# Kernel optimization log

Hardware: AMD Instinct MI355X
Metric: run time of the kernel (lower is better)

## Reference

```python
import jax, jax.numpy as jnp
import numpy as np

N = 100_000      # total nodes (1000 graphs x 100 nodes)
E = 1_600_000    # total edges (avg degree 16)
B = 1_000        # ego nodes == batch size
IN_G, HID, H1, HFC, HMLP = 16, 64, 3, 128, 128
D_SENS, D_TGT, D_AREA = 64, 32, 32
OUT_S, OUT_C = 6, 8


def _seg_softmax(e, dst, n):
    # softmax over incoming edges of each destination node; e: [E,H,1]
    m = jax.ops.segment_max(e, dst, num_segments=n)
    ex = jnp.exp(e - m[dst])
    s = jax.ops.segment_sum(ex, dst, num_segments=n)
    return ex / s[dst]


def _egat(feat, efeat, src, dst, Wni, Wnj, Wfij, Wnode, attn, bias, H, d_node, d_edge):
    # DGL EGATConv: f_out = leaky_relu(f_ni[src] + f_nj[dst] + f_fij + bias)
    n = feat.shape[0]
    f_ni = feat @ Wni.T                      # [N, H*d_edge]
    f_nj = feat @ Wnj.T                      # [N, H*d_edge]
    f_e = efeat @ Wfij.T                     # [E, H*d_edge]
    f_out = f_ni[src] + f_nj[dst] + f_e + bias
    f_out = jax.nn.leaky_relu(f_out, 0.01).reshape(-1, H, d_edge)
    e = (f_out * attn).sum(-1, keepdims=True)   # [E,H,1]
    a = _seg_softmax(e, dst, n)                  # edge softmax by dst
    ft = (feat @ Wnode.T).reshape(n, H, d_node)
    h = jax.ops.segment_sum(ft[src] * a, dst, num_segments=n)  # [N,H,d_node]
    return h, f_out


def _ln(x, gamma, beta, eps=1e-5):
    mu = x.mean(-1, keepdims=True)
    v = ((x - mu) ** 2).mean(-1, keepdims=True)
    return (x - mu) * jax.lax.rsqrt(v + eps) * gamma + beta


def setup_inputs() -> dict:
    key = jax.random.key(0)
    ks = jax.random.split(key, 30)
    ego_idx = jnp.arange(0, N, N // B, dtype=jnp.int32)   # one ego node per graph
    feat = jax.random.normal(ks[0], (N, IN_G), jnp.float32)
    feat = feat.at[:, 5].set(0.0).at[ego_idx, 5].set(1.0)  # ego flag column
    enorm = jax.random.uniform(ks[1], (E, 1), dtype=jnp.float32)
    src = jax.random.randint(ks[2], (E,), 0, N, jnp.int32)
    dst = jax.random.randint(ks[3], (E,), 0, N, jnp.int32)
    sensor = jax.random.normal(ks[4], (B, D_SENS), jnp.float32)
    target = jax.random.normal(ks[5], (B, 1, D_TGT), jnp.float32)
    area = jax.random.normal(ks[6], (B, 1, D_AREA), jnp.float32)

    def w(k, o, i):
        return jax.random.normal(k, (o, i), jnp.float32) / np.sqrt(i).astype(np.float32)

    p = {
        'Wni1': w(ks[7], H1, IN_G), 'Wnj1': w(ks[8], H1, IN_G),
        'Wfij1': w(ks[9], H1, 1), 'Wnode1': w(ks[10], H1 * HID, IN_G),
        'attn1': jax.random.normal(ks[11], (1, H1, 1), jnp.float32),
        'bias1': jnp.zeros((H1,), jnp.float32),
        'Wni3': w(ks[12], 1, H1 * HID), 'Wnj3': w(ks[13], 1, H1 * HID),
        'Wfij3': w(ks[14], 1, H1), 'Wnode3': w(ks[15], HFC, H1 * HID),
        'attn3': jax.random.normal(ks[16], (1, 1, 1), jnp.float32),
        'bias3': jnp.zeros((1,), jnp.float32),
        'Ws1': w(ks[17], HMLP, D_SENS), 'bs1': jnp.zeros((HMLP,), jnp.float32),
        'Ws3': w(ks[18], HFC, HMLP), 'bs3': jnp.zeros((HFC,), jnp.float32),
        'Wt1': w(ks[19], HMLP, D_TGT + D_AREA), 'bt1': jnp.zeros((HMLP,), jnp.float32),
        'Wt2': w(ks[20], HFC, HMLP), 'bt2': jnp.zeros((HFC,), jnp.float32),
        'gM': jnp.ones((HMLP,), jnp.float32), 'bM': jnp.zeros((HMLP,), jnp.float32),
        'gF': jnp.ones((HFC,), jnp.float32), 'bF': jnp.zeros((HFC,), jnp.float32),
        'Wfc': w(ks[21], HFC, 3 * HFC), 'bfc': jnp.zeros((HFC,), jnp.float32),
        'Wst': w(ks[22], OUT_S, HFC), 'bst': jnp.zeros((OUT_S,), jnp.float32),
        'Wca': w(ks[23], OUT_C, HFC), 'bca': jnp.zeros((OUT_C,), jnp.float32),
    }
    return {'feat': feat, 'enorm': enorm, 'sensor': sensor, 'target': target,
            'area': area, 'src': src, 'dst': dst, 'ego_idx': ego_idx, **p}


def reference(feat, enorm, sensor, target, area, src, dst, ego_idx,
              Wni1, Wnj1, Wfij1, Wnode1, attn1, bias1,
              Wni3, Wnj3, Wfij3, Wnode3, attn3, bias3,
              Ws1, bs1, Ws3, bs3, Wt1, bt1, Wt2, bt2,
              gM, bM, gF, bF, Wfc, bfc, Wst, bst, Wca, bca):
    relu = jax.nn.relu
    # --- EGAT stack (dropout p=0 -> identity) ---
    hG, hE = _egat(feat, enorm, src, dst, Wni1, Wnj1, Wfij1, Wnode1, attn1, bias1,
                   H1, HID, 1)
    hG = relu(hG.reshape(-1, H1 * HID))          # [N, 192]
    hE = hE.reshape(-1, H1 * 1)                   # [E, 3]
    hG, hE = _egat(hG, hE, src, dst, Wni3, Wnj3, Wfij3, Wnode3, attn3, bias3,
                   1, HFC, 1)
    hG = relu(hG.reshape(-1, HFC))                # [N, 128]
    hGraph = hG[ego_idx]                          # [B, 128] (feat[:,5]==1 nodes)
    # --- sensor MLP ---
    hS = relu(_ln(sensor @ Ws1.T + bs1, gM, bM))
    hS = relu(_ln(hS @ Ws3.T + bs3, gM, bM))
    # --- target MLP ---
    hTA = jnp.concatenate([target[:, 0, :], area[:, 0, :]], axis=1)  # [B, 64]
    hT = relu(_ln(hTA @ Wt1.T + bt1, gM, bM))
    hT = relu(_ln(hT @ Wt2.T + bt2, gM, bM))
    # --- fusion + heads ---
    h = jnp.concatenate([hGraph, hS, hT], axis=1)  # [B, 384]
    h = relu(_ln(h @ Wfc.T + bfc, gF, bF))
    return (h @ Wst.T + bst, h @ Wca.T + bca)
```

## Files before the change

### kernel.cpp

```cpp
#include <hip/hip_runtime.h>
#include <cstdint>

#define N_NODES 100000
#define N_EDGES 1600000
#define N_BATCH 1000
#define LEAK 0.01f
#define RSTRIDE 64

__device__ __forceinline__ float lrelu(float x){ return x > 0.f ? x : LEAK * x; }
__device__ __forceinline__ float expw(float x){ return __expf(fminf(x, 80.f)); }


__global__ void k_pre(const int* __restrict__ ego, int* __restrict__ egoflag, int* __restrict__ Sflag,
                      const float* __restrict__ feat,
                      const float* __restrict__ Wni1, const float* __restrict__ Wnj1,
                      float4* __restrict__ fni1p, float4* __restrict__ fnj1p){
  int n = blockIdx.x * blockDim.x + threadIdx.x;
  if (n < N_BATCH){ int e = ego[n]; egoflag[e] = 1; Sflag[e] = 1; }
  if (n >= N_NODES) return;
  const float4* f4 = (const float4*)(feat + (size_t)n * 16);
  float4 a = f4[0], b = f4[1], c = f4[2], d = f4[3];
  float f[16] = {a.x,a.y,a.z,a.w, b.x,b.y,b.z,b.w, c.x,c.y,c.z,c.w, d.x,d.y,d.z,d.w};
  float ni[3], nj[3];
  #pragma unroll
  for (int h = 0; h < 3; h++){
    float s0 = 0.f, s1 = 0.f;
    #pragma unroll
    for (int k = 0; k < 16; k++){ s0 += f[k] * Wni1[h * 16 + k]; s1 += f[k] * Wnj1[h * 16 + k]; }
    ni[h] = s0; nj[h] = s1;
  }
  fni1p[n] = make_float4(ni[0], ni[1], ni[2], 0.f);
  fnj1p[n] = make_float4(nj[0], nj[1], nj[2], 0.f);
}

__global__ void k_mark_S(const int* __restrict__ src, const int* __restrict__ dst,
                         const int* __restrict__ egoflag, int* __restrict__ Sflag){
  int e4 = blockIdx.x * blockDim.x + threadIdx.x;
  if (e4 >= N_EDGES / 4) return;
  int4 d = ((const int4*)dst)[e4];
  int f0 = egoflag[d.x], f1 = egoflag[d.y], f2 = egoflag[d.z], f3 = egoflag[d.w];
  if (f0 | f1 | f2 | f3){
    int4 s = ((const int4*)src)[e4];
    if (f0) Sflag[s.x] = 1;
    if (f1) Sflag[s.y] = 1;
    if (f2) Sflag[s.z] = 1;
    if (f3) Sflag[s.w] = 1;
  }
}

__global__ void k_compact(const int* __restrict__ Sflag, int* __restrict__ nodeslot,
                          int* __restrict__ S_ids, int* __restrict__ meta){
  int n = blockIdx.x * blockDim.x + threadIdx.x;
  if (n < N_NODES && Sflag[n]){
    int s = atomicAdd(&meta[0], 1);
    S_ids[s] = n; nodeslot[n] = s + 1;
  }
}

__global__ void k_fill(const int* __restrict__ src, const int* __restrict__ dst,
                       const float* __restrict__ enorm,
                       const int* __restrict__ nodeslot, int* __restrict__ cursor,
                       int2* __restrict__ edata){
  int e4 = blockIdx.x * blockDim.x + threadIdx.x;
  if (e4 >= N_EDGES / 4) return;
  int4 d = ((const int4*)dst)[e4];
  int4 s = ((const int4*)src)[e4];
  float4 en = ((const float4*)enorm)[e4];
  int dd[4] = {d.x, d.y, d.z, d.w};
  int ss[4] = {s.x, s.y, s.z, s.w};
  float ee[4] = {en.x, en.y, en.z, en.w};
  #pragma unroll
  for (int u = 0; u < 4; u++){
    int ns = nodeslot[dd[u]];
    if (ns > 0){
      int sl = ns - 1;
      int p = atomicAdd(&cursor[sl], 1);
      if (p < RSTRIDE) edata[sl * RSTRIDE + p] = make_int2(ss[u], __float_as_int(ee[u]));
    }
  }
}


__global__ __launch_bounds__(256) void k6f(
    const float* __restrict__ feat, const float4* __restrict__ fni1p, const float4* __restrict__ fnj1p,
    const int* __restrict__ S_ids, const int* __restrict__ cursor,
    const int2* __restrict__ edata,
    const float* __restrict__ Wnode1, const float* __restrict__ Wfij1,
    const float* __restrict__ attn1, const float* __restrict__ bias1,
    const float* __restrict__ Wni3, const float* __restrict__ Wnj3,
    const int* __restrict__ meta, float* __restrict__ hG_S,
    float* __restrict__ fni3_S, float* __restrict__ fnj3_S)
{
  __shared__ float Wn1[192 * 17];
  const int t = threadIdx.x;
  for (int i = t; i < 3072; i += 256) Wn1[(i >> 4) * 17 + (i & 15)] = Wnode1[i];
  __syncthreads();
  const int S = meta[0];
  int lane = t & 63;
  int wid = blockIdx.x * 4 + (t >> 6);
  int nw = gridDim.x * 4;
  float wf0 = Wfij1[0], wf1 = Wfij1[1], wf2 = Wfij1[2];
  float at0 = attn1[0], at1 = attn1[1], at2 = attn1[2];
  float b0 = bias1[0], b1 = bias1[1], b2 = bias1[2];
  float wi3a = Wni3[lane], wi3b = Wni3[64 + lane], wi3c = Wni3[128 + lane];
  float wj3a = Wnj3[lane], wj3b = Wnj3[64 + lane], wj3c = Wnj3[128 + lane];
  const int e = lane & 15, cg = lane >> 4;

  for (int s = wid; s < S; s += nw){
    int n = S_ids[s];
    int len = min(cursor[s], RSTRIDE);
    long long j0 = (long long)s * RSTRIDE;
    float4 fj = fnj1p[n];
    float ls0 = 0.f, ls1 = 0.f, ls2 = 0.f;
    float ws[3][4];
    #pragma unroll
    for (int h = 0; h < 3; h++)
      #pragma unroll
      for (int k = 0; k < 4; k++) ws[h][k] = 0.f;

    for (int base = 0; base < len; base += 16){
      int idx = base + e;
      if (idx < len){
        int2 ed = edata[j0 + idx];
        int sn = ed.x; float en = __int_as_float(ed.y);
        float4 fi = fni1p[sn];
        float l0 = lrelu(fi.x + fj.x + en * wf0 + b0);
        float l1 = lrelu(fi.y + fj.y + en * wf1 + b1);
        float l2 = lrelu(fi.z + fj.z + en * wf2 + b2);
        float w0 = expw(l0 * at0), w1 = expw(l1 * at1), w2 = expw(l2 * at2);
        ls0 += w0; ls1 += w1; ls2 += w2;
        const float4 f4 = *(const float4*)(feat + (size_t)sn * 16 + cg * 4);
        float fv[4] = {f4.x, f4.y, f4.z, f4.w};
        #pragma unroll
        for (int k = 0; k < 4; k++){
          ws[0][k] += w0 * fv[k];
          ws[1][k] += w1 * fv[k];
          ws[2][k] += w2 * fv[k];
        }
      }
    }
    #pragma unroll
    for (int off = 1; off < 16; off <<= 1){
      ls0 += __shfl_xor(ls0, off);
      ls1 += __shfl_xor(ls1, off);
      ls2 += __shfl_xor(ls2, off);
      #pragma unroll
      for (int h = 0; h < 3; h++)
        #pragma unroll
        for (int k = 0; k < 4; k++) ws[h][k] += __shfl_xor(ws[h][k], off);
    }
    float inv0 = (len > 0) ? 1.f / ls0 : 0.f;
    float inv1 = (len > 0) ? 1.f / ls1 : 0.f;
    float inv2 = (len > 0) ? 1.f / ls2 : 0.f;
    float aval[3][4];
    #pragma unroll
    for (int k = 0; k < 4; k++){
      aval[0][k] = ws[0][k] * inv0;
      aval[1][k] = ws[1][k] * inv1;
      aval[2][k] = ws[2][k] * inv2;
    }
    float hv[3];
    #pragma unroll
    for (int h = 0; h < 3; h++){
      float acc = 0.f;
      #pragma unroll
      for (int q = 0; q < 4; q++)
        #pragma unroll
        for (int k = 0; k < 4; k++)
          acc += __shfl(aval[h][k], q * 16) * Wn1[(h * 64 + lane) * 17 + q * 4 + k];
      hv[h] = fmaxf(acc, 0.f);
      hG_S[(long long)s * 192 + h * 64 + lane] = hv[h];
    }
    float ni = hv[0] * wi3a + hv[1] * wi3b + hv[2] * wi3c;
    float nj = hv[0] * wj3a + hv[1] * wj3b + hv[2] * wj3c;
    #pragma unroll
    for (int off = 32; off > 0; off >>= 1){
      ni += __shfl_xor(ni, off);
      nj += __shfl_xor(nj, off);
    }
    if (lane == 0){ fni3_S[s] = ni; fnj3_S[s] = nj; }
  }
}


__device__ __forceinline__ void ln2(float& f0, float& f1, float gv, float bv,
                                    float* red, int lane, int wv, int p){
  float a0 = f0, a1 = f1;
  #pragma unroll
  for (int off = 32; off > 0; off >>= 1){ a0 += __shfl_xor(a0, off); a1 += __shfl_xor(a1, off); }
  if (lane == 0){ red[wv * 2] = a0; red[wv * 2 + 1] = a1; }
  __syncthreads();
  float s0 = red[(p * 2) * 2] + red[(p * 2 + 1) * 2];
  float s1 = red[(p * 2) * 2 + 1] + red[(p * 2 + 1) * 2 + 1];
  __syncthreads();
  float d0 = f0 - s0 * (1.f / 128.f), d1 = f1 - s1 * (1.f / 128.f);
  a0 = d0 * d0; a1 = d1 * d1;
  #pragma unroll
  for (int off = 32; off > 0; off >>= 1){ a0 += __shfl_xor(a0, off); a1 += __shfl_xor(a1, off); }
  if (lane == 0){ red[wv * 2] = a0; red[wv * 2 + 1] = a1; }
  __syncthreads();
  float q0 = red[(p * 2) * 2] + red[(p * 2 + 1) * 2];
  float q1 = red[(p * 2) * 2 + 1] + red[(p * 2 + 1) * 2 + 1];
  __syncthreads();
  f0 = fmaxf(0.f, d0 * rsqrtf(q0 * (1.f / 128.f) + 1e-5f) * gv + bv);
  f1 = fmaxf(0.f, d1 * rsqrtf(q1 * (1.f / 128.f) + 1e-5f) * gv + bv);
}

__global__ __launch_bounds__(256) void k8f(
    const int* __restrict__ ego, const int* __restrict__ nodeslot, const int* __restrict__ cursor,
    const int2* __restrict__ edata,
    const float4* __restrict__ fni1p, const float4* __restrict__ fnj1p,
    const float* __restrict__ fni3_S, const float* __restrict__ fnj3_S,
    const float* __restrict__ hG_S, const float* __restrict__ Wnode3,
    const float* __restrict__ Wfij1, const float* __restrict__ attn1, const float* __restrict__ bias1,
    const float* __restrict__ Wfij3, const float* __restrict__ attn3, const float* __restrict__ bias3,
    const float* __restrict__ sensor, const float* __restrict__ target, const float* __restrict__ area,
    const float* __restrict__ Ws1, const float* __restrict__ bs1,
    const float* __restrict__ Ws3, const float* __restrict__ bs3,
    const float* __restrict__ Wt1, const float* __restrict__ bt1,
    const float* __restrict__ Wt2, const float* __restrict__ bt2,
    const float* __restrict__ gM, const float* __restrict__ bM,
    const float* __restrict__ gF, const float* __restrict__ bF,
    const float* __restrict__ Wfc, const float* __restrict__ bfc,
    const float* __restrict__ Wst, const float* __restrict__ bst,
    const float* __restrict__ Wca, const float* __restrict__ bca,
    float* __restrict__ out)
{
  __shared__ float Wl[64 * 130];
  __shared__ float agg[4 * 192];
  __shared__ float xc2[4 * 384];
  __shared__ float act[4 * 64];
  __shared__ float hbuf[4 * 128];
  __shared__ float red[16];
  const int t = threadIdx.x;
  const int lane = t & 63, wv = t >> 6;
  const int o = t & 127, p = t >> 7;
  const int b0 = blockIdx.x * 4;
  const float g_m = gM[o], b_m = bM[o];

  {
    int b = b0 + wv;
    int n = ego[b];
    int slot = nodeslot[n] - 1;
    int len = min(cursor[slot], RSTRIDE);
    long long j0 = (long long)slot * RSTRIDE;
    float wf0 = Wfij1[0], wf1 = Wfij1[1], wf2 = Wfij1[2];
    float bb0 = bias1[0], bb1 = bias1[1], bb2 = bias1[2];
    float g0 = Wfij3[0], g1 = Wfij3[1], g2 = Wfij3[2];
    float at3 = attn3[0], bb3 = bias3[0];
    float4 fj = fnj1p[n];
    float fnj3v = fnj3_S[slot];

    float lsum = 0.f;
    float acc[3] = {0.f, 0.f, 0.f};
    for (int base = 0; base < len; base += 64){
      int j = base + lane;
      float w = 0.f; int ss = 0;
      if (j < len){
        int2 ed = edata[j0 + j];
        int sn = ed.x; float en = __int_as_float(ed.y);
        float4 fi = fni1p[sn];
        float l0 = lrelu(fi.x + fj.x + en * wf0 + bb0);
        float l1 = lrelu(fi.y + fj.y + en * wf1 + bb1);
        float l2 = lrelu(fi.z + fj.z + en * wf2 + bb2);
        float fe3 = l0 * g0 + l1 * g1 + l2 * g2;
        ss = nodeslot[sn] - 1;
        float l3 = lrelu(fni3_S[ss] + fnj3v + fe3 + bb3);
        w = expw(l3 * at3);
        lsum += w;
      }
      int c2 = min(64, len - base);
      for (int i0 = 0; i0 < c2; i0 += 4){
        float wvv[4], fr[4][3];
        #pragma unroll
        for (int u = 0; u < 4; u++){
          int idx = i0 + u;
          int s2 = __shfl(ss, idx);
          wvv[u] = __shfl(w, idx);
          bool ok = idx < c2;
          #pragma unroll
          for (int r = 0; r < 3; r++)
            fr[u][r] = ok ? hG_S[(long long)s2 * 192 + r * 64 + lane] : 0.f;
          if (!ok) wvv[u] = 0.f;
        }
        #pragma unroll
        for (int u = 0; u < 4; u++)
          #pragma unroll
          for (int r = 0; r < 3; r++) acc[r] += wvv[u] * fr[u][r];
      }
    }
    #pragma unroll
    for (int off = 32; off > 0; off >>= 1) lsum += __shfl_xor(lsum, off);
    float inv = (len > 0) ? 1.f / lsum : 0.f;
    #pragma unroll
    for (int r = 0; r < 3; r++) agg[wv * 192 + r * 64 + lane] = acc[r] * inv;
  }

  {
    for (int i = t; i < 256; i += 256){
      int r = i >> 6, c = i & 63;
      act[i] = sensor[(b0 + r) * 64 + c];
    }
    __syncthreads();
    for (int i = t; i < 128 * 64; i += 256){
      int oo = i >> 6, cc = i & 63;
      Wl[cc * 130 + oo] = Ws1[i];
    }
    __syncthreads();
    float z0 = bs1[o], z1 = z0;
    #pragma unroll 8
    for (int c = 0; c < 64; c++){
      float w = Wl[c * 130 + o];
      z0 += w * act[p * 64 + c];
      z1 += w * act[(p + 2) * 64 + c];
    }
    ln2(z0, z1, g_m, b_m, red, lane, wv, p);
    hbuf[p * 128 + o] = z0; hbuf[(p + 2) * 128 + o] = z1;
    __syncthreads();
    z0 = bs3[o]; z1 = z0;
    for (int ch = 0; ch < 2; ch++){
      for (int i = t; i < 128 * 64; i += 256){
        int oo = i >> 6, cc = i & 63;
        Wl[cc * 130 + oo] = Ws3[oo * 128 + ch * 64 + cc];
      }
      __syncthreads();
      #pragma unroll 8
      for (int c = 0; c < 64; c++){
        float w = Wl[c * 130 + o];
        z0 += w * hbuf[p * 128 + ch * 64 + c];
        z1 += w * hbuf[(p + 2) * 128 + ch * 64 + c];
      }
      __syncthreads();
    }
    ln2(z0, z1, g_m, b_m, red, lane, wv, p);
    xc2[p * 384 + 128 + o] = z0; xc2[(p + 2) * 384 + 128 + o] = z1;
  }

  {
    for (int i = t; i < 256; i += 256){
      int r = i >> 6, c = i & 63;
      act[i] = (c < 32) ? target[(b0 + r) * 32 + c] : area[(b0 + r) * 32 + c - 32];
    }
    __syncthreads();
    for (int i = t; i < 128 * 64; i += 256){
      int oo = i >> 6, cc = i & 63;
      Wl[cc * 130 + oo] = Wt1[i];
    }
    __syncthreads();
    float z0 = bt1[o], z1 = z0;
    #pragma unroll 8
    for (int c = 0; c < 64; c++){
      float w = Wl[c * 130 + o];
      z0 += w * act[p * 64 + c];
      z1 += w * act[(p + 2) * 64 + c];
    }
    ln2(z0, z1, g_m, b_m, red, lane, wv, p);
    hbuf[p * 128 + o] = z0; hbuf[(p + 2) * 128 + o] = z1;
    __syncthreads();
    z0 = bt2[o]; z1 = z0;
    for (int ch = 0; ch < 2; ch++){
      for (int i = t; i < 128 * 64; i += 256){
        int oo = i >> 6, cc = i & 63;
        Wl[cc * 130 + oo] = Wt2[oo * 128 + ch * 64 + cc];
      }
      __syncthreads();
      #pragma unroll 8
      for (int c = 0; c < 64; c++){
        float w = Wl[c * 130 + o];
        z0 += w * hbuf[p * 128 + ch * 64 + c];
        z1 += w * hbuf[(p + 2) * 128 + ch * 64 + c];
      }
      __syncthreads();
    }
    ln2(z0, z1, g_m, b_m, red, lane, wv, p);
    xc2[p * 384 + 256 + o] = z0; xc2[(p + 2) * 384 + 256 + o] = z1;
  }
  __syncthreads();

  {
    float h0 = 0.f, h1 = 0.f;
    for (int ch = 0; ch < 3; ch++){
      for (int i = t; i < 128 * 64; i += 256){
        int oo = i >> 6, cc = i & 63;
        Wl[cc * 130 + oo] = Wnode3[oo * 192 + ch * 64 + cc];
      }
      __syncthreads();
      #pragma unroll 8
      for (int c = 0; c < 64; c++){
        float w = Wl[c * 130 + o];
        h0 += w * agg[p * 192 + ch * 64 + c];
        h1 += w * agg[(p + 2) * 192 + ch * 64 + c];
      }
      __syncthreads();
    }
    xc2[p * 384 + o] = fmaxf(0.f, h0);
    xc2[(p + 2) * 384 + o] = fmaxf(0.f, h1);
    __syncthreads();
  }

  float f0 = bfc[o], f1 = f0;
  for (int ch = 0; ch < 6; ch++){
    for (int i = t; i < 128 * 64; i += 256){
      int oo = i >> 6, cc = i & 63;
      Wl[cc * 130 + oo] = Wfc[oo * 384 + ch * 64 + cc];
    }
    __syncthreads();
    #pragma unroll 8
    for (int c = 0; c < 64; c++){
      float w = Wl[c * 130 + o];
      f0 += w * xc2[p * 384 + ch * 64 + c];
      f1 += w * xc2[(p + 2) * 384 + ch * 64 + c];
    }
    __syncthreads();
  }
  ln2(f0, f1, gF[o], bF[o], red, lane, wv, p);

  float* v1 = agg;
  v1[p * 128 + o] = f0;
  v1[(p + 2) * 128 + o] = f1;
  for (int i = t; i < 14 * 128; i += 256){
    int oo = i >> 7, cc = i & 127;
    Wl[cc * 15 + oo] = (oo < 6) ? Wst[oo * 128 + cc] : Wca[(oo - 6) * 128 + cc];
  }
  __syncthreads();
  if (o < 14){
    float bb = (o < 6) ? bst[o] : bca[o - 6];
    float a0 = bb, a1 = bb;
    #pragma unroll 8
    for (int c = 0; c < 128; c++){
      float w = Wl[c * 15 + o];
      a0 += w * v1[p * 128 + c];
      a1 += w * v1[(p + 2) * 128 + c];
    }
    int e0 = b0 + p, e1 = e0 + 2;
    if (o < 6){
      out[e0 * 6 + o] = a0;
      out[e1 * 6 + o] = a1;
    } else {
      out[N_BATCH * 6 + e0 * 8 + o - 6] = a0;
      out[N_BATCH * 6 + e1 * 8 + o - 6] = a1;
    }
  }
}


extern "C" void kernel_launch(void* const* d_in, const int* in_sizes, int n_in,
                              void* d_out, int out_size, void* d_ws, size_t ws_size,
                              hipStream_t stream)
{
  const float* feat   = (const float*)d_in[0];
  const float* enorm  = (const float*)d_in[1];
  const float* sensor = (const float*)d_in[2];
  const float* target = (const float*)d_in[3];
  const float* area   = (const float*)d_in[4];
  const int*   src    = (const int*)d_in[5];
  const int*   dst    = (const int*)d_in[6];
  const int*   ego    = (const int*)d_in[7];
  const float* Wni1   = (const float*)d_in[8];
  const float* Wnj1   = (const float*)d_in[9];
  const float* Wfij1  = (const float*)d_in[10];
  const float* Wnode1 = (const float*)d_in[11];
  const float* attn1  = (const float*)d_in[12];
  const float* bias1  = (const float*)d_in[13];
  const float* Wni3   = (const float*)d_in[14];
  const float* Wnj3   = (const float*)d_in[15];
  const float* Wfij3  = (const float*)d_in[16];
  const float* Wnode3 = (const float*)d_in[17];
  const float* attn3  = (const float*)d_in[18];
  const float* bias3  = (const float*)d_in[19];
  const float* Ws1    = (const float*)d_in[20];
  const float* bs1    = (const float*)d_in[21];
  const float* Ws3    = (const float*)d_in[22];
  const float* bs3    = (const float*)d_in[23];
  const float* Wt1    = (const float*)d_in[24];
  const float* bt1    = (const float*)d_in[25];
  const float* Wt2    = (const float*)d_in[26];
  const float* bt2    = (const float*)d_in[27];
  const float* gM     = (const float*)d_in[28];
  const float* bM     = (const float*)d_in[29];
  const float* gF     = (const float*)d_in[30];
  const float* bF     = (const float*)d_in[31];
  const float* Wfc    = (const float*)d_in[32];
  const float* bfc    = (const float*)d_in[33];
  const float* Wst    = (const float*)d_in[34];
  const float* bst    = (const float*)d_in[35];
  const float* Wca    = (const float*)d_in[36];
  const float* bca    = (const float*)d_in[37];
  float* out = (float*)d_out;

  char* ws = (char*)d_ws;
  size_t off = 0;
  auto alloc = [&](size_t bytes) -> size_t {
    size_t o = off;
    off = (off + bytes + 255) & ~(size_t)255;
    return o;
  };

  size_t o_meta    = alloc(256);
  size_t o_egoflag = alloc((size_t)N_NODES * 4);
  size_t o_Sflag   = alloc((size_t)N_NODES * 4);
  size_t o_nodeslot= alloc((size_t)N_NODES * 4);
  size_t o_cursor  = alloc((size_t)N_NODES * 4);
  size_t zero_bytes = off;
  size_t o_fni1p   = alloc((size_t)N_NODES * 16);
  size_t o_fnj1p   = alloc((size_t)N_NODES * 16);
  size_t o_S_ids   = alloc((size_t)N_NODES * 4);
  size_t o_fni3    = alloc((size_t)N_NODES * 4);
  size_t o_fnj3    = alloc((size_t)N_NODES * 4);
  size_t rem = (ws_size > off) ? ws_size - off : 0;
  size_t scap = rem / (RSTRIDE * 8 + 768);
  if (scap > (size_t)N_NODES) scap = N_NODES;
  if (scap < 1) scap = 1;
  size_t o_edata = alloc(scap * RSTRIDE * 8);
  size_t o_hG_S  = alloc(scap * 768);

  int*    meta      = (int*)(ws + o_meta);
  int*    egoflag   = (int*)(ws + o_egoflag);
  int*    Sflag     = (int*)(ws + o_Sflag);
  int*    nodeslot  = (int*)(ws + o_nodeslot);
  int*    cursor    = (int*)(ws + o_cursor);
  float4* fni1p     = (float4*)(ws + o_fni1p);
  float4* fnj1p     = (float4*)(ws + o_fnj1p);
  int*    S_ids     = (int*)(ws + o_S_ids);
  float*  fni3_S    = (float*)(ws + o_fni3);
  float*  fnj3_S    = (float*)(ws + o_fnj3);
  int2*   edata     = (int2*)(ws + o_edata);
  float*  hG_S      = (float*)(ws + o_hG_S);

  hipMemsetAsync(ws, 0, zero_bytes, stream);

  k_pre<<<(N_NODES + 255) / 256, 256, 0, stream>>>(ego, egoflag, Sflag, feat, Wni1, Wnj1, fni1p, fnj1p);
  k_mark_S<<<(N_EDGES / 4 + 255) / 256, 256, 0, stream>>>(src, dst, egoflag, Sflag);
  k_compact<<<(N_NODES + 255) / 256, 256, 0, stream>>>(Sflag, nodeslot, S_ids, meta);
  k_fill<<<(N_EDGES / 4 + 255) / 256, 256, 0, stream>>>(src, dst, enorm, nodeslot, cursor, edata);
  k6f<<<2048, 256, 0, stream>>>(feat, fni1p, fnj1p, S_ids, cursor, edata,
                                Wnode1, Wfij1, attn1, bias1, Wni3, Wnj3, meta,
                                hG_S, fni3_S, fnj3_S);
  k8f<<<N_BATCH / 4, 256, 0, stream>>>(ego, nodeslot, cursor, edata, fni1p, fnj1p,
                                       fni3_S, fnj3_S, hG_S, Wnode3,
                                       Wfij1, attn1, bias1, Wfij3, attn3, bias3,
                                       sensor, target, area, Ws1, bs1, Ws3, bs3,
                                       Wt1, bt1, Wt2, bt2, gM, bM,
                                       gF, bF, Wfc, bfc, Wst, bst, Wca, bca, out);
  (void)in_sizes; (void)n_in; (void)out_size;
}
```

Baseline: 278.7 us.

## Merge node precompute into edge-mark kernel and halve batch rows per head block

The ego-flag writes move into a tiny separate kernel. The per-node projection and the edge-marking pass now share one launch, split by block index. The fused head kernel k8f now handles 2 batch rows per block instead of 4, so it launches twice as many blocks with less register and LDS state per thread. The aim is to cut launch count and raise parallelism in the tail kernel, at the cost of staging the MLP weights into LDS twice as often in total.

```diff
diff --git a/kernel.cpp b/kernel.cpp
--- a/kernel.cpp
+++ b/kernel.cpp
@@ -6,36 +6,41 @@
 #define N_BATCH 1000
 #define LEAK 0.01f
 #define RSTRIDE 64
+#define PREB 391
 
 __device__ __forceinline__ float lrelu(float x){ return x > 0.f ? x : LEAK * x; }
 __device__ __forceinline__ float expw(float x){ return __expf(fminf(x, 80.f)); }
 
 
-__global__ void k_pre(const int* __restrict__ ego, int* __restrict__ egoflag, int* __restrict__ Sflag,
-                      const float* __restrict__ feat,
-                      const float* __restrict__ Wni1, const float* __restrict__ Wnj1,
-                      float4* __restrict__ fni1p, float4* __restrict__ fnj1p){
-  int n = blockIdx.x * blockDim.x + threadIdx.x;
-  if (n < N_BATCH){ int e = ego[n]; egoflag[e] = 1; Sflag[e] = 1; }
-  if (n >= N_NODES) return;
-  const float4* f4 = (const float4*)(feat + (size_t)n * 16);
-  float4 a = f4[0], b = f4[1], c = f4[2], d = f4[3];
-  float f[16] = {a.x,a.y,a.z,a.w, b.x,b.y,b.z,b.w, c.x,c.y,c.z,c.w, d.x,d.y,d.z,d.w};
-  float ni[3], nj[3];
-  #pragma unroll
-  for (int h = 0; h < 3; h++){
-    float s0 = 0.f, s1 = 0.f;
-    #pragma unroll
-    for (int k = 0; k < 16; k++){ s0 += f[k] * Wni1[h * 16 + k]; s1 += f[k] * Wnj1[h * 16 + k]; }
-    ni[h] = s0; nj[h] = s1;
-  }
-  fni1p[n] = make_float4(ni[0], ni[1], ni[2], 0.f);
-  fnj1p[n] = make_float4(nj[0], nj[1], nj[2], 0.f);
-}
-
-__global__ void k_mark_S(const int* __restrict__ src, const int* __restrict__ dst,
-                         const int* __restrict__ egoflag, int* __restrict__ Sflag){
-  int e4 = blockIdx.x * blockDim.x + threadIdx.x;
+__global__ void k_ego(const int* __restrict__ ego, int* __restrict__ egoflag, int* __restrict__ Sflag){
+  int i = blockIdx.x * blockDim.x + threadIdx.x;
+  if (i < N_BATCH){ int n = ego[i]; egoflag[n] = 1; Sflag[n] = 1; }
+}
+
+__global__ void k_mark_pre(const int* __restrict__ src, const int* __restrict__ dst,
+                           const int* __restrict__ egoflag, int* __restrict__ Sflag,
+                           const float* __restrict__ feat,
+                           const float* __restrict__ Wni1, const float* __restrict__ Wnj1,
+                           float4* __restrict__ fni1p, float4* __restrict__ fnj1p){
+  if (blockIdx.x < PREB){
+    int n = blockIdx.x * 256 + threadIdx.x;
+    if (n >= N_NODES) return;
+    const float4* f4 = (const float4*)(feat + (size_t)n * 16);
+    float4 a = f4[0], b = f4[1], c = f4[2], d = f4[3];
+    float f[16] = {a.x,a.y,a.z,a.w, b.x,b.y,b.z,b.w, c.x,c.y,c.z,c.w, d.x,d.y,d.z,d.w};
+    float ni[3], nj[3];
+    #pragma unroll
+    for (int h = 0; h < 3; h++){
+      float s0 = 0.f, s1 = 0.f;
+      #pragma unroll
+      for (int k = 0; k < 16; k++){ s0 += f[k] * Wni1[h * 16 + k]; s1 += f[k] * Wnj1[h * 16 + k]; }
+      ni[h] = s0; nj[h] = s1;
+    }
+    fni1p[n] = make_float4(ni[0], ni[1], ni[2], 0.f);
+    fnj1p[n] = make_float4(nj[0], nj[1], nj[2], 0.f);
+    return;
+  }
+  int e4 = (blockIdx.x - PREB) * 256 + threadIdx.x;
   if (e4 >= N_EDGES / 4) return;
   int4 d = ((const int4*)dst)[e4];
   int f0 = egoflag[d.x], f1 = egoflag[d.y], f2 = egoflag[d.z], f3 = egoflag[d.w];
@@ -183,27 +188,23 @@
 }
 
 
-__device__ __forceinline__ void ln2(float& f0, float& f1, float gv, float bv,
-                                    float* red, int lane, int wv, int p){
-  float a0 = f0, a1 = f1;
+__device__ __forceinline__ void ln1(float& f0, float gv, float bv, float* red, int lane, int wv, int p){
+  float a0 = f0;
   #pragma unroll
-  for (int off = 32; off > 0; off >>= 1){ a0 += __shfl_xor(a0, off); a1 += __shfl_xor(a1, off); }
-  if (lane == 0){ red[wv * 2] = a0; red[wv * 2 + 1] = a1; }
-  __syncthreads();
-  float s0 = red[(p * 2) * 2] + red[(p * 2 + 1) * 2];
-  float s1 = red[(p * 2) * 2 + 1] + red[(p * 2 + 1) * 2 + 1];
-  __syncthreads();
-  float d0 = f0 - s0 * (1.f / 128.f), d1 = f1 - s1 * (1.f / 128.f);
-  a0 = d0 * d0; a1 = d1 * d1;
+  for (int off = 32; off > 0; off >>= 1) a0 += __shfl_xor(a0, off);
+  if (lane == 0) red[wv] = a0;
+  __syncthreads();
+  float s0 = red[2 * p] + red[2 * p + 1];
+  __syncthreads();
+  float d0 = f0 - s0 * (1.f / 128.f);
+  a0 = d0 * d0;
   #pragma unroll
-  for (int off = 32; off > 0; off >>= 1){ a0 += __shfl_xor(a0, off); a1 += __shfl_xor(a1, off); }
-  if (lane == 0){ red[wv * 2] = a0; red[wv * 2 + 1] = a1; }
-  __syncthreads();
-  float q0 = red[(p * 2) * 2] + red[(p * 2 + 1) * 2];
-  float q1 = red[(p * 2) * 2 + 1] + red[(p * 2 + 1) * 2 + 1];
+  for (int off = 32; off > 0; off >>= 1) a0 += __shfl_xor(a0, off);
+  if (lane == 0) red[wv] = a0;
+  __syncthreads();
+  float q0 = red[2 * p] + red[2 * p + 1];
   __syncthreads();
   f0 = fmaxf(0.f, d0 * rsqrtf(q0 * (1.f / 128.f) + 1e-5f) * gv + bv);
-  f1 = fmaxf(0.f, d1 * rsqrtf(q1 * (1.f / 128.f) + 1e-5f) * gv + bv);
 }
 
 __global__ __launch_bounds__(256) void k8f(
@@ -226,19 +227,19 @@
     const float* __restrict__ Wca, const float* __restrict__ bca,
     float* __restrict__ out)
 {
-  __shared__ float Wl[64 * 130];
-  __shared__ float agg[4 * 192];
-  __shared__ float xc2[4 * 384];
-  __shared__ float act[4 * 64];
-  __shared__ float hbuf[4 * 128];
-  __shared__ float red[16];
+  __shared__ float Wl[64 * 129];
+  __shared__ float agg[2 * 192];
+  __shared__ float xc2[2 * 384];
+  __shared__ float act[2 * 64];
+  __shared__ float hbuf[2 * 128];
+  __shared__ float red[8];
   const int t = threadIdx.x;
   const int lane = t & 63, wv = t >> 6;
   const int o = t & 127, p = t >> 7;
-  const int b0 = blockIdx.x * 4;
+  const int b0 = blockIdx.x * 2;
   const float g_m = gM[o], b_m = bM[o];
 
-  {
+  if (wv < 2){
     int b = b0 + wv;
     int n = ego[b];
     int slot = nodeslot[n] - 1;
@@ -297,149 +298,113 @@
   }
 
   {
-    for (int i = t; i < 256; i += 256){
+    for (int i = t; i < 128; i += 256){
       int r = i >> 6, c = i & 63;
       act[i] = sensor[(b0 + r) * 64 + c];
     }
     __syncthreads();
     for (int i = t; i < 128 * 64; i += 256){
       int oo = i >> 6, cc = i & 63;
-      Wl[cc * 130 + oo] = Ws1[i];
-    }
-    __syncthreads();
-    float z0 = bs1[o], z1 = z0;
+      Wl[cc * 129 + oo] = Ws1[i];
+    }
+    __syncthreads();
+    float z0 = bs1[o];
     #pragma unroll 8
-    for (int c = 0; c < 64; c++){
-      float w = Wl[c * 130 + o];
-      z0 += w * act[p * 64 + c];
-      z1 += w * act[(p + 2) * 64 + c];
-    }
-    ln2(z0, z1, g_m, b_m, red, lane, wv, p);
-    hbuf[p * 128 + o] = z0; hbuf[(p + 2) * 128 + o] = z1;
-    __syncthreads();
-    z0 = bs3[o]; z1 = z0;
+    for (int c = 0; c < 64; c++) z0 += Wl[c * 129 + o] * act[p * 64 + c];
+    ln1(z0, g_m, b_m, red, lane, wv, p);
+    hbuf[p * 128 + o] = z0;
+    __syncthreads();
+    z0 = bs3[o];
     for (int ch = 0; ch < 2; ch++){
       for (int i = t; i < 128 * 64; i += 256){
         int oo = i >> 6, cc = i & 63;
-        Wl[cc * 130 + oo] = Ws3[oo * 128 + ch * 64 + cc];
+        Wl[cc * 129 + oo] = Ws3[oo * 128 + ch * 64 + cc];
       }
       __syncthreads();
       #pragma unroll 8
-      for (int c = 0; c < 64; c++){
-        float w = Wl[c * 130 + o];
-        z0 += w * hbuf[p * 128 + ch * 64 + c];
-        z1 += w * hbuf[(p + 2) * 128 + ch * 64 + c];
-      }
+      for (int c = 0; c < 64; c++) z0 += Wl[c * 129 + o] * hbuf[p * 128 + ch * 64 + c];
       __syncthreads();
     }
-    ln2(z0, z1, g_m, b_m, red, lane, wv, p);
-    xc2[p * 384 + 128 + o] = z0; xc2[(p + 2) * 384 + 128 + o] = z1;
+    ln1(z0, g_m, b_m, red, lane, wv, p);
+    xc2[p * 384 + 128 + o] = z0;
   }
 
   {
-    for (int i = t; i < 256; i += 256){
+    for (int i = t; i < 128; i += 256){
       int r = i >> 6, c = i & 63;
       act[i] = (c < 32) ? target[(b0 + r) * 32 + c] : area[(b0 + r) * 32 + c - 32];
     }
     __syncthreads();
     for (int i = t; i < 128 * 64; i += 256){
       int oo = i >> 6, cc = i & 63;
-      Wl[cc * 130 + oo] = Wt1[i];
-    }
-    __syncthreads();
-    float z0 = bt1[o], z1 = z0;
+      Wl[cc * 129 + oo] = Wt1[i];
+    }
+    __syncthreads();
+    float z0 = bt1[o];
     #pragma unroll 8
-    for (int c = 0; c < 64; c++){
-      float w = Wl[c * 130 + o];
-      z0 += w * act[p * 64 + c];
-      z1 += w * act[(p + 2) * 64 + c];
-    }
-    ln2(z0, z1, g_m, b_m, red, lane, wv, p);
-    hbuf[p * 128 + o] = z0; hbuf[(p + 2) * 128 + o] = z1;
-    __syncthreads();
-    z0 = bt2[o]; z1 = z0;
+    for (int c = 0; c < 64; c++) z0 += Wl[c * 129 + o] * act[p * 64 + c];
+    ln1(z0, g_m, b_m, red, lane, wv, p);
+    hbuf[p * 128 + o] = z0;
+    __syncthreads();
+    z0 = bt2[o];
     for (int ch = 0; ch < 2; ch++){
       for (int i = t; i < 128 * 64; i += 256){
         int oo = i >> 6, cc = i & 63;
-        Wl[cc * 130 + oo] = Wt2[oo * 128 + ch * 64 + cc];
+        Wl[cc * 129 + oo] = Wt2[oo * 128 + ch * 64 + cc];
       }
       __syncthreads();
       #pragma unroll 8
-      for (int c = 0; c < 64; c++){
-        float w = Wl[c * 130 + o];
-        z0 += w * hbuf[p * 128 + ch * 64 + c];
-        z1 += w * hbuf[(p + 2) * 128 + ch * 64 + c];
-      }
+      for (int c = 0; c < 64; c++) z0 += Wl[c * 129 + o] * hbuf[p * 128 + ch * 64 + c];
       __syncthreads();
     }
-    ln2(z0, z1, g_m, b_m, red, lane, wv, p);
-    xc2[p * 384 + 256 + o] = z0; xc2[(p + 2) * 384 + 256 + o] = z1;
+    ln1(z0, g_m, b_m, red, lane, wv, p);
+    xc2[p * 384 + 256 + o] = z0;
   }
   __syncthreads();
 
   {
-    float h0 = 0.f, h1 = 0.f;
+    float h0 = 0.f;
     for (int ch = 0; ch < 3; ch++){
       for (int i = t; i < 128 * 64; i += 256){
         int oo = i >> 6, cc = i & 63;
-        Wl[cc * 130 + oo] = Wnode3[oo * 192 + ch * 64 + cc];
+        Wl[cc * 129 + oo] = Wnode3[oo * 192 + ch * 64 + cc];
       }
       __syncthreads();
       #pragma unroll 8
-      for (int c = 0; c < 64; c++){
-        float w = Wl[c * 130 + o];
-        h0 += w * agg[p * 192 + ch * 64 + c];
-        h1 += w * agg[(p + 2) * 192 + ch * 64 + c];
-      }
+      for (int c = 0; c < 64; c++) h0 += Wl[c * 129 + o] * agg[p * 192 + ch * 64 + c];
       __syncthreads();
     }
     xc2[p * 384 + o] = fmaxf(0.f, h0);
-    xc2[(p + 2) * 384 + o] = fmaxf(0.f, h1);
-    __syncthreads();
-  }
-
-  float f0 = bfc[o], f1 = f0;
+    __syncthreads();
+  }
+
+  float f0 = bfc[o];
   for (int ch = 0; ch < 6; ch++){
     for (int i = t; i < 128 * 64; i += 256){
       int oo = i >> 6, cc = i & 63;
-      Wl[cc * 130 + oo] = Wfc[oo * 384 + ch * 64 + cc];
+      Wl[cc * 129 + oo] = Wfc[oo * 384 + ch * 64 + cc];
     }
     __syncthreads();
     #pragma unroll 8
-    for (int c = 0; c < 64; c++){
-      float w = Wl[c * 130 + o];
-      f0 += w * xc2[p * 384 + ch * 64 + c];
-      f1 += w * xc2[(p + 2) * 384 + ch * 64 + c];
-    }
-    __syncthreads();
-  }
-  ln2(f0, f1, gF[o], bF[o], red, lane, wv, p);
+    for (int c = 0; c < 64; c++) f0 += Wl[c * 129 + o] * xc2[p * 384 + ch * 64 + c];
+    __syncthreads();
+  }
+  ln1(f0, gF[o], bF[o], red, lane, wv, p);
 
   float* v1 = agg;
   v1[p * 128 + o] = f0;
-  v1[(p + 2) * 128 + o] = f1;
   for (int i = t; i < 14 * 128; i += 256){
     int oo = i >> 7, cc = i & 127;
     Wl[cc * 15 + oo] = (oo < 6) ? Wst[oo * 128 + cc] : Wca[(oo - 6) * 128 + cc];
   }
   __syncthreads();
   if (o < 14){
-    float bb = (o < 6) ? bst[o] : bca[o - 6];
-    float a0 = bb, a1 = bb;
+    float a0 = (o < 6) ? bst[o] : bca[o - 6];
     #pragma unroll 8
-    for (int c = 0; c < 128; c++){
-      float w = Wl[c * 15 + o];
-      a0 += w * v1[p * 128 + c];
-      a1 += w * v1[(p + 2) * 128 + c];
-    }
-    int e0 = b0 + p, e1 = e0 + 2;
-    if (o < 6){
-      out[e0 * 6 + o] = a0;
-      out[e1 * 6 + o] = a1;
-    } else {
-      out[N_BATCH * 6 + e0 * 8 + o - 6] = a0;
-      out[N_BATCH * 6 + e1 * 8 + o - 6] = a1;
-    }
+    for (int c = 0; c < 128; c++) a0 += Wl[c * 15 + o] * v1[p * 128 + c];
+    int e0 = b0 + p;
+    if (o < 6) out[e0 * 6 + o] = a0;
+    else       out[N_BATCH * 6 + e0 * 8 + o - 6] = a0;
   }
 }
 
@@ -529,14 +494,15 @@
 
   hipMemsetAsync(ws, 0, zero_bytes, stream);
 
-  k_pre<<<(N_NODES + 255) / 256, 256, 0, stream>>>(ego, egoflag, Sflag, feat, Wni1, Wnj1, fni1p, fnj1p);
-  k_mark_S<<<(N_EDGES / 4 + 255) / 256, 256, 0, stream>>>(src, dst, egoflag, Sflag);
+  k_ego<<<(N_BATCH + 255) / 256, 256, 0, stream>>>(ego, egoflag, Sflag);
+  k_mark_pre<<<PREB + (N_EDGES / 4 + 255) / 256, 256, 0, stream>>>(
+      src, dst, egoflag, Sflag, feat, Wni1, Wnj1, fni1p, fnj1p);
   k_compact<<<(N_NODES + 255) / 256, 256, 0, stream>>>(Sflag, nodeslot, S_ids, meta);
   k_fill<<<(N_EDGES / 4 + 255) / 256, 256, 0, stream>>>(src, dst, enorm, nodeslot, cursor, edata);
   k6f<<<2048, 256, 0, stream>>>(feat, fni1p, fnj1p, S_ids, cursor, edata,
                                 Wnode1, Wfij1, attn1, bias1, Wni3, Wnj3, meta,
                                 hG_S, fni3_S, fnj3_S);
-  k8f<<<N_BATCH / 4, 256, 0, stream>>>(ego, nodeslot, cursor, edata, fni1p, fnj1p,
+  k8f<<<N_BATCH / 2, 256, 0, stream>>>(ego, nodeslot, cursor, edata, fni1p, fnj1p,
                                        fni3_S, fnj3_S, hG_S, Wnode3,
                                        Wfij1, attn1, bias1, Wfij3, attn3, bias3,
                                        sensor, target, area, Ws1, bs1, Ws3, bs3,
```

After: 272.5 us. 1.02x faster.
